# Optimization experiments

Hardware: AMD Instinct MI355X
Metric: run time of the kernel (lower is better)

Reference implementation:

```python
import jax, jax.numpy as jnp
import numpy as np

B, DIM, H, W = 8, 64, 128, 128
HEADS = 8
HID = DIM * 2          # ffn_expansion_factor = 2
DCONV = DIM // 4       # partial-conv channels
EPS_LN = 1e-5
EPS_NRM = 1e-12

def _conv(x, w, groups=1):
    # stride-1 conv, SAME padding (matches padding=1 for k=3, padding=0 for k=1)
    return jax.lax.conv_general_dilated(
        x, w, (1, 1), 'SAME',
        dimension_numbers=('NCHW', 'OIHW', 'NCHW'),
        feature_group_count=groups)

def _ln_channel(x, w, b):
    # WithBias LayerNorm over channel dim (to_3d puts c last, normalize last dim)
    mu = x.mean(axis=1, keepdims=True)
    var = ((x - mu) ** 2).mean(axis=1, keepdims=True)
    return (x - mu) / jnp.sqrt(var + EPS_LN) * w[None, :, None, None] + b[None, :, None, None]

def setup_inputs() -> dict:
    key = jax.random.key(0)
    ks = jax.random.split(key, 8)
    s = 0.02
    return {
        'x': jax.random.normal(ks[0], (B, DIM, H, W), jnp.float32),
        'ln1_w': jnp.ones((DIM,), jnp.float32),
        'ln1_b': jnp.zeros((DIM,), jnp.float32),
        'qkv_w': jax.random.normal(ks[1], (3 * DIM, DIM, 1, 1), jnp.float32) * s,
        'qkv_dw_w': jax.random.normal(ks[2], (3 * DIM, 1, 3, 3), jnp.float32) * s,
        'temperature': jnp.ones((HEADS, 1, 1), jnp.float32),
        'attn_mix': jnp.ones((2,), jnp.float32),
        'proj_w': jax.random.normal(ks[3], (DIM, DIM, 1, 1), jnp.float32) * s,
        'ln2_w': jnp.ones((DIM,), jnp.float32),
        'ln2_b': jnp.zeros((DIM,), jnp.float32),
        'pconv_w': jax.random.normal(ks[4], (DCONV, DCONV, 3, 3), jnp.float32) * s,
        'pin_w': jax.random.normal(ks[5], (2 * HID, DIM, 1, 1), jnp.float32) * s,
        'dw_w': jax.random.normal(ks[6], (HID, 1, 3, 3), jnp.float32) * s,
        'pout_w': jax.random.normal(ks[7], (DIM, HID, 1, 1), jnp.float32) * s,
    }

def reference(x, ln1_w, ln1_b, qkv_w, qkv_dw_w, temperature, attn_mix,
              proj_w, ln2_w, ln2_b, pconv_w, pin_w, dw_w, pout_w):
    b, c, h, w = x.shape
    ch = c // HEADS
    # ---- TwinPeakAttention on norm1(x) ----
    y = _ln_channel(x, ln1_w, ln1_b)
    qkv = _conv(_conv(y, qkv_w), qkv_dw_w, groups=3 * c)
    q, k, v = jnp.split(qkv, 3, axis=1)
    rs = lambda t: t.reshape(b, HEADS, ch, h * w)          # b head c (h w)
    q, k, v = rs(q), rs(k), rs(v)
    q = q / jnp.maximum(jnp.linalg.norm(q, axis=-1, keepdims=True), EPS_NRM)
    k = k / jnp.maximum(jnp.linalg.norm(k, axis=-1, keepdims=True), EPS_NRM)
    scores = jnp.einsum('bhcn,bhdn->bhcd', q, k)           # [b, head, ch, ch]
    attn_sm = jax.nn.softmax(scores * temperature[None], axis=-1)
    attn_relu = jnp.maximum(scores, 0.0) ** 2
    wmix = jax.nn.softmax(attn_mix)
    attn = wmix[0] * attn_sm + wmix[1] * attn_relu
    out = jnp.einsum('bhcd,bhdn->bhcn', attn, v).reshape(b, c, h, w)
    x = x + _conv(out, proj_w)
    # ---- FDFN on norm2(x) ----
    y = _ln_channel(x, ln2_w, ln2_b)
    y = jnp.concatenate([_conv(y[:, :DCONV], pconv_w), y[:, DCONV:]], axis=1)
    y = _conv(y, pin_w)                                    # [b, 2*HID, h, w]
    a, g = jnp.split(y, 2, axis=1)
    a = _conv(a, dw_w, groups=HID)
    y = _conv(jax.nn.gelu(a, approximate=False) * g, pout_w)
    return x + y
```

## Files before the change

kernel.cpp:

```cpp
#include <hip/hip_runtime.h>
#include <math.h>

#define NPIX 16384
#define B_ 8

typedef __attribute__((ext_vector_type(4))) float f32x4;
typedef __attribute__((ext_vector_type(8))) short bf16x8;
typedef __attribute__((ext_vector_type(4))) unsigned int u32x4;

__device__ inline unsigned short f2bf(float f) {
  unsigned int u = __builtin_bit_cast(unsigned int, f);
  return (unsigned short)((u + 0x7fffu + ((u >> 16) & 1u)) >> 16);
}
__device__ inline float bf2f(unsigned short h) {
  unsigned int u = ((unsigned int)h) << 16;
  return __builtin_bit_cast(float, u);
}
__device__ inline unsigned int pack2(unsigned short a, unsigned short b) {
  return (unsigned int)a | ((unsigned int)b << 16);
}
__device__ inline f32x4 mfma16(bf16x8 a, bf16x8 b, f32x4 c) {
  return __builtin_amdgcn_mfma_f32_16x16x32_bf16(a, b, c, 0, 0, 0);
}
__device__ inline void unpack8(u32x4 u, float* f) {
#pragma unroll
  for (int i = 0; i < 4; ++i) {
    unsigned int w = u[i];
    f[2 * i]     = __builtin_bit_cast(float, w << 16);
    f[2 * i + 1] = __builtin_bit_cast(float, w & 0xffff0000u);
  }
}


__global__ __launch_bounds__(256) void k0_prep(
    const float* __restrict__ wq, const float* __restrict__ lw,
    const float* __restrict__ lb, const float* __restrict__ pin,
    const float* __restrict__ pout, unsigned short* __restrict__ wq2,
    float* __restrict__ s1, float* __restrict__ s2,
    unsigned short* __restrict__ pinb, unsigned short* __restrict__ pob) {
  int bid = blockIdx.x, t = threadIdx.x;
  if (bid == 0) {
    if (t < 192) {
      int co = t;
      float a = 0.f, bsum = 0.f;
      for (int ci = 0; ci < 64; ++ci) {
        float w = wq[co * 64 + ci];
        unsigned short hb = f2bf(w * lw[ci]);
        wq2[co * 64 + ci] = hb;
        a += bf2f(hb);
        bsum = fmaf(w, lb[ci], bsum);
      }
      s1[co] = a;
      s2[co] = bsum;
    }
  } else if (bid <= 64) {
    int i = (bid - 1) * 256 + t;
    pinb[i] = f2bf(pin[i]);
  } else {
    int i = (bid - 65) * 256 + t;
    pob[i] = f2bf(pout[i]);
  }
}

__global__ __launch_bounds__(256) void k1_qkv(
    const float* __restrict__ x, const unsigned short* __restrict__ wq2,
    const float* __restrict__ s1, const float* __restrict__ s2,
    unsigned short* __restrict__ qkv) {
  __shared__ __align__(16) unsigned char lx[64 * 128];
  __shared__ float sumL[4][64], sqL[4][64], muL[64], rsL[64];
  __shared__ __align__(16) unsigned short epi[4][16][72];
  int t = threadIdx.x, blk = blockIdx.x;
  int b = blk >> 8, hw0 = (blk & 255) * 64;
  const float* xb = x + (size_t)b * 64 * NPIX + hw0;
  int p = t & 63, g8 = t >> 6;
  float psum = 0.f, psq = 0.f;
#pragma unroll
  for (int r = 0; r < 2; ++r) {
    int ci0 = g8 * 8 + r * 32;
    float v[8];
#pragma unroll
    for (int j = 0; j < 8; ++j) {
      v[j] = xb[(size_t)(ci0 + j) * NPIX + p];
      psum += v[j];
      psq = fmaf(v[j], v[j], psq);
    }
    u32x4 pk;
#pragma unroll
    for (int j = 0; j < 4; ++j) pk[j] = pack2(f2bf(v[2 * j]), f2bf(v[2 * j + 1]));
    unsigned int addr = ((unsigned)(p * 128 + ci0 * 2)) ^ ((p & 7) << 4);
    *(u32x4*)&lx[addr] = pk;
  }
  sumL[g8][p] = psum;
  sqL[g8][p] = psq;
  __syncthreads();
  if (t < 64) {
    float s = sumL[0][t] + sumL[1][t] + sumL[2][t] + sumL[3][t];
    float q = sqL[0][t] + sqL[1][t] + sqL[2][t] + sqL[3][t];
    float mu = s * (1.f / 64.f);
    float var = q * (1.f / 64.f) - mu * mu;
    muL[t] = mu;
    rsL[t] = rsqrtf(fmaxf(var, 0.f) + 1e-5f);
  }
  __syncthreads();
  int lane = t & 63, wv = t >> 6, l16 = lane & 15, g = lane >> 4;
  int co0 = wv * 48;
  bf16x8 A[3][2];
#pragma unroll
  for (int ct = 0; ct < 3; ++ct) {
    int co = co0 + ct * 16 + l16;
#pragma unroll
    for (int kh = 0; kh < 2; ++kh)
      A[ct][kh] = *(const bf16x8*)(wq2 + (size_t)co * 64 + kh * 32 + g * 8);
  }
  f32x4 acc[3][4];
#pragma unroll
  for (int ct = 0; ct < 3; ++ct)
#pragma unroll
    for (int nt = 0; nt < 4; ++nt) acc[ct][nt] = (f32x4)0.f;
#pragma unroll
  for (int nt = 0; nt < 4; ++nt) {
    int pp = nt * 16 + l16;
#pragma unroll
    for (int kh = 0; kh < 2; ++kh) {
      unsigned int addr = ((unsigned)(pp * 128 + (kh * 32 + g * 8) * 2)) ^ ((pp & 7) << 4);
      bf16x8 Bf = *(const bf16x8*)&lx[addr];
#pragma unroll
      for (int ct = 0; ct < 3; ++ct) acc[ct][nt] = mfma16(A[ct][kh], Bf, acc[ct][nt]);
    }
  }
  int row1 = hw0 >> 7, wb1 = hw0 & 127;
  unsigned short* ob = qkv + ((size_t)(b * 128 + row1) * 192) * 128 + wb1;
#pragma unroll
  for (int ct = 0; ct < 3; ++ct) {
#pragma unroll
    for (int r = 0; r < 4; ++r) {
      int co = co0 + ct * 16 + g * 4 + r;
      float s1v = s1[co], s2v = s2[co];
#pragma unroll
      for (int nt = 0; nt < 4; ++nt) {
        int pl = nt * 16 + l16;
        float val = (acc[ct][nt][r] - muL[pl] * s1v) * rsL[pl] + s2v;
        epi[wv][g * 4 + r][pl] = f2bf(val);
      }
    }
#pragma unroll
    for (int i = 0; i < 2; ++i) {
      int chunk = i * 64 + lane, co_l = chunk >> 3, oct = chunk & 7;
      u32x4 v = *(const u32x4*)&epi[wv][co_l][oct * 8];
      *(u32x4*)(ob + (size_t)(co0 + ct * 16 + co_l) * 128 + oct * 8) = v;
    }
  }
}

__global__ __launch_bounds__(256) void k2_dw3x3(
    const unsigned short* __restrict__ in, const float* __restrict__ w9,
    unsigned short* __restrict__ out) {
  int blk0 = blockIdx.x;
  int blk = (blk0 & 7) * 1536 + (blk0 >> 3);
  int id = blk * 256 + threadIdx.x;
  int oct = id & 15;
  int cr = id >> 4;
  int ch = cr % 192;
  int br = cr / 192;
  int row = br & 127;
  int w0 = oct * 8;
  const float* wp = w9 + ch * 9;
  float wgt[9];
#pragma unroll
  for (int j = 0; j < 9; ++j) wgt[j] = wp[j];
  float rowv[3][10];
#pragma unroll
  for (int dy = 0; dy < 3; ++dy) {
#pragma unroll
    for (int i = 0; i < 10; ++i) rowv[dy][i] = 0.f;
    int hh = row + dy - 1;
    if ((unsigned)hh < 128u) {
      const unsigned short* rp = in + ((size_t)(br + dy - 1) * 192 + ch) * 128 + w0;
      u32x4 m = *(const u32x4*)rp;
      unpack8(m, &rowv[dy][1]);
      if (w0 > 0) rowv[dy][0] = bf2f(rp[-1]);
      if (w0 < 120) rowv[dy][9] = bf2f(rp[8]);
    }
  }
  u32x4 res;
#pragma unroll
  for (int i = 0; i < 8; i += 2) {
    float a0 = 0.f, a1 = 0.f;
#pragma unroll
    for (int dy = 0; dy < 3; ++dy)
#pragma unroll
      for (int dx = 0; dx < 3; ++dx) {
        a0 = fmaf(wgt[dy * 3 + dx], rowv[dy][i + dx], a0);
        a1 = fmaf(wgt[dy * 3 + dx], rowv[dy][i + 1 + dx], a1);
      }
    res[i >> 1] = pack2(f2bf(a0), f2bf(a1));
  }
  *(u32x4*)(out + ((size_t)br * 192 + ch) * 128 + w0) = res;
}

__global__ __launch_bounds__(256) void k3a_mfma(
    const unsigned short* __restrict__ qkvd, float* __restrict__ parts) {
  __shared__ float red[4][640];
  int blk = blockIdx.x;
  int b = blk >> 6, chunk = blk & 63;
  int t = threadIdx.x;
  int lane = t & 63, wv = t >> 6, l16 = lane & 15, g = lane >> 4;
  const unsigned short* bb = qkvd + (size_t)(b * 128) * 192 * 128;
  int n0 = chunk * 256 + wv * 64;
  f32x4 S[4], QQ[4], KK[4];
#pragma unroll
  for (int i = 0; i < 4; ++i) { S[i] = (f32x4)0.f; QQ[i] = (f32x4)0.f; KK[i] = (f32x4)0.f; }
#pragma unroll
  for (int ks = 0; ks < 2; ++ks) {
    int k0 = n0 + ks * 32 + g * 8;
    int r = k0 >> 7, w = k0 & 127;
    const unsigned short* rowb = bb + ((size_t)r * 192) * 128 + w;
    bf16x8 Q[4], K[4];
#pragma unroll
    for (int t4 = 0; t4 < 4; ++t4) {
      Q[t4] = *(const bf16x8*)(rowb + (size_t)(t4 * 16 + l16) * 128);
      K[t4] = *(const bf16x8*)(rowb + (size_t)(64 + t4 * 16 + l16) * 128);
    }
#pragma unroll
    for (int t4 = 0; t4 < 4; ++t4) {
      S[t4]  = mfma16(Q[t4], K[t4], S[t4]);
      QQ[t4] = mfma16(Q[t4], Q[t4], QQ[t4]);
      KK[t4] = mfma16(K[t4], K[t4], KK[t4]);
    }
  }
  int hi = l16 >> 3;
#pragma unroll
  for (int t4 = 0; t4 < 4; ++t4) {
#pragma unroll
    for (int r = 0; r < 4; ++r) {
      int m = g * 4 + r;
      if ((m >> 3) == hi) {
        int head = 2 * t4 + hi;
        red[wv][head * 80 + 16 + (m & 7) * 8 + (l16 & 7)] = S[t4][r];
      }
      if (m == l16) {
        int c = t4 * 16 + l16;
        red[wv][(c >> 3) * 80 + (c & 7)] = QQ[t4][r];
        red[wv][(c >> 3) * 80 + 8 + (c & 7)] = KK[t4][r];
      }
    }
  }
  __syncthreads();
  float* pb = parts + (size_t)blk * 640;
  for (int i = t; i < 640; i += 256)
    pb[i] = red[0][i] + red[1][i] + red[2][i] + red[3][i];
}

__global__ __launch_bounds__(256) void k3bc(
    const float* __restrict__ parts, const float* __restrict__ temp,
    const float* __restrict__ mix, const float* __restrict__ pw,
    unsigned short* __restrict__ M) {
  int b = blockIdx.x, t = threadIdx.x;
  __shared__ float s[8][80];
  __shared__ float att[8][64];
  for (int i = t; i < 640; i += 256) {
    const float* pbase = parts + (size_t)b * 64 * 640 + i;
    float v = 0.f;
    for (int c = 0; c < 64; ++c) v += pbase[c * 640];
    s[i / 80][i % 80] = v;
  }
  __syncthreads();
  float m0 = fmaxf(mix[0], mix[1]);
  float e0 = expf(mix[0] - m0), e1 = expf(mix[1] - m0);
  float w0 = e0 / (e0 + e1), w1 = e1 / (e0 + e1);
  for (int i = t; i < 512; i += 256) {
    int head = i >> 6, e = i & 63, c = e >> 3, d = e & 7;
    float tt = temp[head];
    float rq = 1.f / fmaxf(sqrtf(s[head][c]), 1e-12f);
    float sc[8];
    float mx = -1e30f;
#pragma unroll
    for (int d2 = 0; d2 < 8; ++d2) {
      float rk = 1.f / fmaxf(sqrtf(s[head][8 + d2]), 1e-12f);
      sc[d2] = s[head][16 + c * 8 + d2] * rq * rk;
      mx = fmaxf(mx, sc[d2] * tt);
    }
    float sum = 0.f;
#pragma unroll
    for (int d2 = 0; d2 < 8; ++d2) sum += expf(sc[d2] * tt - mx);
    float sm = expf(sc[d] * tt - mx) / sum;
    float r = fmaxf(sc[d], 0.f);
    r = r * r;
    att[head][e] = w0 * sm + w1 * r;
  }
  __syncthreads();
  for (int i = t; i < 4096; i += 256) {
    int co = i >> 6, ci = i & 63, head = ci >> 3, d = ci & 7;
    float a = 0.f;
#pragma unroll
    for (int cc = 0; cc < 8; ++cc)
      a = fmaf(pw[co * 64 + head * 8 + cc], att[head][cc * 8 + d], a);
    M[(size_t)b * 4096 + i] = f2bf(a);
  }
}

__global__ __launch_bounds__(256) void k4_av(
    const unsigned short* __restrict__ qkvd, const unsigned short* __restrict__ Mb,
    const float* __restrict__ x, const float* __restrict__ lw,
    const float* __restrict__ lb, unsigned short* __restrict__ x1,
    unsigned short* __restrict__ y2) {
  __shared__ __align__(16) unsigned char lv[64 * 128];
  __shared__ float sumL[4][64], sqL[4][64], muL[64], rsL[64];
  int t = threadIdx.x, blk = blockIdx.x;
  int b = blk >> 8, hw0 = (blk & 255) * 64;
  int row4 = hw0 >> 7, wb4 = hw0 & 127;
  const unsigned short* vb = qkvd + ((size_t)(b * 128 + row4) * 192 + 128) * 128 + wb4;
  int p = t & 63, g8 = t >> 6;
#pragma unroll
  for (int r = 0; r < 2; ++r) {
    int ci0 = g8 * 8 + r * 32;
    unsigned short hh[8];
#pragma unroll
    for (int j = 0; j < 8; ++j) hh[j] = vb[(size_t)(ci0 + j) * 128 + p];
    u32x4 pk;
#pragma unroll
    for (int j = 0; j < 4; ++j) pk[j] = pack2(hh[2 * j], hh[2 * j + 1]);
    unsigned int addr = ((unsigned)(p * 128 + ci0 * 2)) ^ ((p & 7) << 4);
    *(u32x4*)&lv[addr] = pk;
  }
  __syncthreads();
  int lane = t & 63, wv = t >> 6, l16 = lane & 15, g = lane >> 4;
  bf16x8 A[2];
#pragma unroll
  for (int kh = 0; kh < 2; ++kh)
    A[kh] = *(const bf16x8*)(Mb + (size_t)b * 4096 + (size_t)(wv * 16 + l16) * 64 + kh * 32 + g * 8);
  f32x4 acc[4];
#pragma unroll
  for (int nt = 0; nt < 4; ++nt) acc[nt] = (f32x4)0.f;
#pragma unroll
  for (int nt = 0; nt < 4; ++nt) {
    int pp = nt * 16 + l16;
#pragma unroll
    for (int kh = 0; kh < 2; ++kh) {
      unsigned int addr = ((unsigned)(pp * 128 + (kh * 32 + g * 8) * 2)) ^ ((pp & 7) << 4);
      bf16x8 Bf = *(const bf16x8*)&lv[addr];
      acc[nt] = mfma16(A[kh], Bf, acc[nt]);
    }
  }
  const float* xb = x + (size_t)b * 64 * NPIX + hw0;
  unsigned short* x1b = x1 + (size_t)b * 64 * NPIX + hw0;
  float vals[4][4];
#pragma unroll
  for (int nt = 0; nt < 4; ++nt) {
    float ps = 0.f, pq = 0.f;
#pragma unroll
    for (int r = 0; r < 4; ++r) {
      int co = wv * 16 + g * 4 + r;
      size_t idx = (size_t)co * NPIX + nt * 16 + l16;
      float a = acc[nt][r] + xb[idx];
      vals[nt][r] = a;
      x1b[idx] = f2bf(a);
      ps += a;
      pq = fmaf(a, a, pq);
    }
    ps += __shfl_xor(ps, 16); ps += __shfl_xor(ps, 32);
    pq += __shfl_xor(pq, 16); pq += __shfl_xor(pq, 32);
    if (g == 0) { sumL[wv][nt * 16 + l16] = ps; sqL[wv][nt * 16 + l16] = pq; }
  }
  __syncthreads();
  if (t < 64) {
    float s = sumL[0][t] + sumL[1][t] + sumL[2][t] + sumL[3][t];
    float q = sqL[0][t] + sqL[1][t] + sqL[2][t] + sqL[3][t];
    float mu = s * (1.f / 64.f);
    float var = q * (1.f / 64.f) - mu * mu;
    muL[t] = mu;
    rsL[t] = rsqrtf(fmaxf(var, 0.f) + 1e-5f);
  }
  __syncthreads();
  unsigned short* y2b = y2 + (size_t)b * 64 * NPIX + hw0;
#pragma unroll
  for (int nt = 0; nt < 4; ++nt)
#pragma unroll
    for (int r = 0; r < 4; ++r) {
      int co = wv * 16 + g * 4 + r;
      int pl = nt * 16 + l16;
      float yv = (vals[nt][r] - muL[pl]) * rsL[pl] * lw[co] + lb[co];
      y2b[(size_t)co * NPIX + pl] = f2bf(yv);
    }
}

__global__ __launch_bounds__(256) void k5_pconv(
    const unsigned short* __restrict__ y2, const float* __restrict__ pcw,
    unsigned short* __restrict__ pc) {
  __shared__ unsigned short ly[16 * 120];
  int t = threadIdx.x, blk = blockIdx.x;
  int b = blk >> 8, tile = blk & 255;
  int ty = tile >> 4, tx = tile & 15;
  int h0 = ty * 8, w0 = tx * 8;
  const unsigned short* yb = y2 + (size_t)b * 64 * NPIX;
  for (int i = t; i < 1600; i += 256) {
    int ci = i / 100, r = i - ci * 100;
    int hy = r / 10, hx = r - hy * 10;
    int gh = h0 - 1 + hy, gw = w0 - 1 + hx;
    unsigned short v = 0;
    if ((unsigned)gh < 128u && (unsigned)gw < 128u) v = yb[(size_t)ci * NPIX + gh * 128 + gw];
    ly[ci * 120 + hy * 12 + hx] = v;
  }
  __syncthreads();
  int lp = t & 63;
  int py = lp >> 3, px = lp & 7;
  int cq = __builtin_amdgcn_readfirstlane(t >> 6);
  int co0 = cq * 4;
  float a0 = 0.f, a1 = 0.f, a2 = 0.f, a3 = 0.f;
  for (int ci = 0; ci < 16; ++ci) {
    float nb[9];
#pragma unroll
    for (int ky = 0; ky < 3; ++ky)
#pragma unroll
      for (int kx = 0; kx < 3; ++kx)
        nb[ky * 3 + kx] = bf2f(ly[ci * 120 + (py + ky) * 12 + px + kx]);
    const float* wp = pcw + (co0 * 16 + ci) * 9;
#pragma unroll
    for (int k = 0; k < 9; ++k) {
      a0 = fmaf(wp[k],       nb[k], a0);
      a1 = fmaf(wp[144 + k], nb[k], a1);
      a2 = fmaf(wp[288 + k], nb[k], a2);
      a3 = fmaf(wp[432 + k], nb[k], a3);
    }
  }
  size_t obase = (size_t)b * 16 * NPIX + (h0 + py) * 128 + w0 + px;
  pc[obase + (size_t)(co0 + 0) * NPIX] = f2bf(a0);
  pc[obase + (size_t)(co0 + 1) * NPIX] = f2bf(a1);
  pc[obase + (size_t)(co0 + 2) * NPIX] = f2bf(a2);
  pc[obase + (size_t)(co0 + 3) * NPIX] = f2bf(a3);
}

__global__ __launch_bounds__(256) void k6_pin(
    const unsigned short* __restrict__ pc, const unsigned short* __restrict__ y2,
    const unsigned short* __restrict__ pinb, unsigned short* __restrict__ ag) {
  __shared__ __align__(16) unsigned char bt[64 * 128];
  __shared__ __align__(16) unsigned short epi[4][16][72];
  int t = threadIdx.x, blk = blockIdx.x;
  int b = blk >> 8, hw0 = (blk & 255) * 64;
  int px = t & 63, cb = t >> 6;
  {
    const unsigned short* base = (cb == 0) ? (pc + (size_t)b * 16 * NPIX)
                                           : (y2 + (size_t)b * 64 * NPIX);
#pragma unroll
    for (int j = 0; j < 16; j += 2) {
      int ch = cb * 16 + j;
      unsigned short v0 = base[(size_t)ch * NPIX + hw0 + px];
      unsigned short v1 = base[(size_t)(ch + 1) * NPIX + hw0 + px];
      unsigned int addr = ((unsigned)(px * 128 + ch * 2)) ^ ((px & 7) << 4);
      *(unsigned int*)&bt[addr] = pack2(v0, v1);
    }
  }
  __syncthreads();
  int lane = t & 63, wv = t >> 6, l16 = lane & 15, g = lane >> 4;
  bf16x8 A[4][2];
#pragma unroll
  for (int ct = 0; ct < 4; ++ct) {
    int co = wv * 64 + ct * 16 + l16;
#pragma unroll
    for (int kh = 0; kh < 2; ++kh)
      A[ct][kh] = *(const bf16x8*)(pinb + (size_t)co * 64 + kh * 32 + g * 8);
  }
  f32x4 acc[4][4];
#pragma unroll
  for (int ct = 0; ct < 4; ++ct)
#pragma unroll
    for (int nt = 0; nt < 4; ++nt) acc[ct][nt] = (f32x4)0.f;
#pragma unroll
  for (int nt = 0; nt < 4; ++nt) {
    int pp = nt * 16 + l16;
#pragma unroll
    for (int kh = 0; kh < 2; ++kh) {
      unsigned int addr = ((unsigned)(pp * 128 + (kh * 32 + g * 8) * 2)) ^ ((pp & 7) << 4);
      bf16x8 Bf = *(const bf16x8*)&bt[addr];
#pragma unroll
      for (int ct = 0; ct < 4; ++ct) acc[ct][nt] = mfma16(A[ct][kh], Bf, acc[ct][nt]);
    }
  }
  int row6 = hw0 >> 7, wb6 = hw0 & 127;
  unsigned short* ab = ag + ((size_t)(b * 128 + row6) * 256) * 128 + wb6;
#pragma unroll
  for (int ct = 0; ct < 4; ++ct) {
#pragma unroll
    for (int nt = 0; nt < 4; ++nt)
#pragma unroll
      for (int r = 0; r < 4; ++r)
        epi[wv][g * 4 + r][nt * 16 + l16] = f2bf(acc[ct][nt][r]);
#pragma unroll
    for (int i = 0; i < 2; ++i) {
      int chunk = i * 64 + lane, co_l = chunk >> 3, oct = chunk & 7;
      u32x4 v = *(const u32x4*)&epi[wv][co_l][oct * 8];
      int co = wv * 64 + ct * 16 + co_l;
      *(u32x4*)(ab + (size_t)co * 128 + oct * 8) = v;
    }
  }
}

__global__ __launch_bounds__(256) void k7_fdfn(
    const unsigned short* __restrict__ ag, const float* __restrict__ dww,
    const unsigned short* __restrict__ pob, const unsigned short* __restrict__ x1,
    float* __restrict__ out) {
  __shared__ __align__(16) unsigned char bt[32 * 256];
  __shared__ float dwl[1152];
  int t = threadIdx.x;
  int blk0 = blockIdx.x;
  int blk = (blk0 & 7) * 512 + (blk0 >> 3);
  int b = blk >> 9, rr = blk & 511;
  int row = rr >> 2, w0t = (rr & 3) * 32;
  for (int i = t; i < 1152; i += 256) dwl[i] = dww[i];

  int chp = t >> 2, oct = t & 3;
  int ch0 = chp * 2;
  int w0 = w0t + oct * 8;
  bool hasL = (w0 > 0), hasR = (w0 < 120);
  u32x4 arow[2][3];
  u32x4 grow[2];
  unsigned short eL[2][3], eR[2][3];
#pragma unroll
  for (int cc = 0; cc < 2; ++cc) {
    int ch = ch0 + cc;
    grow[cc] = *(const u32x4*)(ag + ((size_t)(b * 128 + row) * 256 + 128 + ch) * 128 + w0);
#pragma unroll
    for (int dy = 0; dy < 3; ++dy) {
      int hh = row + dy - 1;
      bool v = (unsigned)hh < 128u;
      const unsigned short* rp = ag + ((size_t)(b * 128 + hh) * 256 + ch) * 128 + w0;
      arow[cc][dy] = v ? *(const u32x4*)rp : (u32x4)0u;
      eL[cc][dy] = (v && hasL) ? rp[-1] : (unsigned short)0;
      eR[cc][dy] = (v && hasR) ? rp[8] : (unsigned short)0;
    }
  }
  __syncthreads();

  {
    unsigned short hv[2][8];
#pragma unroll
    for (int cc = 0; cc < 2; ++cc) {
      float rowa[3][10], gt[8];
#pragma unroll
      for (int dy = 0; dy < 3; ++dy) {
        rowa[dy][0] = bf2f(eL[cc][dy]);
        unpack8(arow[cc][dy], &rowa[dy][1]);
        rowa[dy][9] = bf2f(eR[cc][dy]);
      }
      unpack8(grow[cc], gt);
      float wgt[9];
#pragma unroll
      for (int j = 0; j < 9; ++j) wgt[j] = dwl[(ch0 + cc) * 9 + j];
#pragma unroll
      for (int i2 = 0; i2 < 8; ++i2) {
        float a = 0.f;
#pragma unroll
        for (int dy = 0; dy < 3; ++dy)
#pragma unroll
          for (int dx = 0; dx < 3; ++dx)
            a = fmaf(wgt[dy * 3 + dx], rowa[dy][i2 + dx], a);
        float gl = 0.5f * a * (1.f + erff(a * 0.70710678118654752f)) * gt[i2];
        hv[cc][i2] = f2bf(gl);
      }
    }
#pragma unroll
    for (int i2 = 0; i2 < 8; ++i2) {
      int pxl = oct * 8 + i2;
      unsigned int f = (unsigned)(((pxl & 7) ^ (pxl >> 3)) << 4);
      unsigned int addr = (unsigned)(pxl * 256) + (((unsigned)(ch0 * 2)) ^ f);
      *(unsigned int*)&bt[addr] = pack2(hv[0][i2], hv[1][i2]);
    }
  }
  __syncthreads();
  int lane = t & 63, wv = t >> 6, l16 = lane & 15, g = lane >> 4;
  bf16x8 A[4];
#pragma unroll
  for (int kh = 0; kh < 4; ++kh)
    A[kh] = *(const bf16x8*)(pob + (size_t)(wv * 16 + l16) * 128 + kh * 32 + g * 8);
  f32x4 acc[2];
#pragma unroll
  for (int nt = 0; nt < 2; ++nt) acc[nt] = (f32x4)0.f;
#pragma unroll
  for (int nt = 0; nt < 2; ++nt) {
    int pp = nt * 16 + l16;
    unsigned int f = (unsigned)(((pp & 7) ^ (pp >> 3)) << 4);
#pragma unroll
    for (int kh = 0; kh < 4; ++kh) {
      unsigned int addr = (unsigned)(pp * 256) + (((unsigned)((kh * 32 + g * 8) * 2)) ^ f);
      bf16x8 Bf = *(const bf16x8*)&bt[addr];
      acc[nt] = mfma16(A[kh], Bf, acc[nt]);
    }
  }
  __syncthreads();
  float* ebuf = (float*)&bt[wv * 2048];
#pragma unroll
  for (int nt = 0; nt < 2; ++nt)
#pragma unroll
    for (int r = 0; r < 4; ++r)
      ebuf[(g * 4 + r) * 32 + nt * 16 + l16] = acc[nt][r];
  const unsigned short* x1b = x1 + (size_t)b * 64 * NPIX + row * 128 + w0t;
  float* ob = out + (size_t)b * 64 * NPIX + row * 128 + w0t;
#pragma unroll
  for (int i = 0; i < 2; ++i) {
    int chunk = i * 64 + lane;
    int co_l = chunk >> 3, q4 = (chunk & 7) * 4;
    f32x4 v = *(const f32x4*)&ebuf[co_l * 32 + q4];
    int co = wv * 16 + co_l;
    uint2 xv = *(const uint2*)(x1b + (size_t)co * NPIX + q4);
    f32x4 o;
    o[0] = v[0] + bf2f((unsigned short)(xv.x & 0xffffu));
    o[1] = v[1] + bf2f((unsigned short)(xv.x >> 16));
    o[2] = v[2] + bf2f((unsigned short)(xv.y & 0xffffu));
    o[3] = v[3] + bf2f((unsigned short)(xv.y >> 16));
    *(f32x4*)(ob + (size_t)co * NPIX + q4) = o;
  }
}

extern "C" void kernel_launch(void* const* d_in, const int* in_sizes, int n_in,
                              void* d_out, int out_size, void* d_ws, size_t ws_size,
                              hipStream_t stream) {
  const float* x       = (const float*)d_in[0];
  const float* ln1_w   = (const float*)d_in[1];
  const float* ln1_b   = (const float*)d_in[2];
  const float* qkv_w   = (const float*)d_in[3];
  const float* qkv_dww = (const float*)d_in[4];
  const float* temp    = (const float*)d_in[5];
  const float* mix     = (const float*)d_in[6];
  const float* proj_w  = (const float*)d_in[7];
  const float* ln2_w   = (const float*)d_in[8];
  const float* ln2_b   = (const float*)d_in[9];
  const float* pconv_w = (const float*)d_in[10];
  const float* pin_w   = (const float*)d_in[11];
  const float* dw_w    = (const float*)d_in[12];
  const float* pout_w  = (const float*)d_in[13];
  float* out = (float*)d_out;

  if (ws_size < (size_t)117515776) return;
  char* w8 = (char*)d_ws;
  unsigned short* qkv  = (unsigned short*)(w8 + 0);
  unsigned short* qkvd = (unsigned short*)(w8 + 50331648);
  unsigned short* x1   = (unsigned short*)(w8 + 100663296);
  unsigned short* wq2  = (unsigned short*)(w8 + 117440512);
  float*          s1   = (float*)(w8 + 117465088);
  float*          s2   = (float*)(w8 + 117465856);
  unsigned short* pinb = (unsigned short*)(w8 + 117466624);
  unsigned short* pob  = (unsigned short*)(w8 + 117499392);
  float*          parts= (float*)(w8 + 0);
  unsigned short* M    = (unsigned short*)(w8 + 2097152);
  unsigned short* y2   = (unsigned short*)(w8 + 4194304);
  unsigned short* pc   = (unsigned short*)(w8 + 20971520);
  unsigned short* ag   = (unsigned short*)(w8 + 33554432);

  k0_prep<<<97, 256, 0, stream>>>(qkv_w, ln1_w, ln1_b, pin_w, pout_w, wq2, s1, s2, pinb, pob);
  k1_qkv<<<2048, 256, 0, stream>>>(x, wq2, s1, s2, qkv);
  k2_dw3x3<<<12288, 256, 0, stream>>>(qkv, qkv_dww, qkvd);
  k3a_mfma<<<512, 256, 0, stream>>>(qkvd, parts);
  k3bc<<<8, 256, 0, stream>>>(parts, temp, mix, proj_w, M);
  k4_av<<<2048, 256, 0, stream>>>(qkvd, M, x, ln2_w, ln2_b, x1, y2);
  k5_pconv<<<2048, 256, 0, stream>>>(y2, pconv_w, pc);
  k6_pin<<<2048, 256, 0, stream>>>(pc, y2, pinb, ag);
  k7_fdfn<<<4096, 256, 0, stream>>>(ag, dw_w, pob, x1, out);
}
```

Before: 184.9 us.

## Stage k4 outputs through LDS for vector stores; widen k7 tiles to 64 pixels

In k4_av, the bf16 x1 and y2 outputs were written as scattered 2-byte stores. They are now staged in a padded LDS epilogue buffer and written back as 16-byte rows per channel. k7_fdfn moves to 512-thread blocks covering 64 pixels per row, with eight waves split across output-channel tiles and pixel halves. This halves the grid and amortizes the depthwise weight load. The cost is more LDS per block and possibly lower occupancy for k7.

```diff
diff --git a/kernel.cpp b/kernel.cpp
--- a/kernel.cpp
+++ b/kernel.cpp
@@ -306,6 +306,7 @@
     unsigned short* __restrict__ y2) {
   __shared__ __align__(16) unsigned char lv[64 * 128];
   __shared__ float sumL[4][64], sqL[4][64], muL[64], rsL[64];
+  __shared__ __align__(16) unsigned short epi[4][16][72];
   int t = threadIdx.x, blk = blockIdx.x;
   int b = blk >> 8, hw0 = (blk & 255) * 64;
   int row4 = hw0 >> 7, wb4 = hw0 & 127;
@@ -354,13 +355,19 @@
       size_t idx = (size_t)co * NPIX + nt * 16 + l16;
       float a = acc[nt][r] + xb[idx];
       vals[nt][r] = a;
-      x1b[idx] = f2bf(a);
+      epi[wv][g * 4 + r][nt * 16 + l16] = f2bf(a);
       ps += a;
       pq = fmaf(a, a, pq);
     }
     ps += __shfl_xor(ps, 16); ps += __shfl_xor(ps, 32);
     pq += __shfl_xor(pq, 16); pq += __shfl_xor(pq, 32);
     if (g == 0) { sumL[wv][nt * 16 + l16] = ps; sqL[wv][nt * 16 + l16] = pq; }
+  }
+#pragma unroll
+  for (int i = 0; i < 2; ++i) {
+    int chunk = i * 64 + lane, co_l = chunk >> 3, oct = chunk & 7;
+    u32x4 v = *(const u32x4*)&epi[wv][co_l][oct * 8];
+    *(u32x4*)(x1b + (size_t)(wv * 16 + co_l) * NPIX + oct * 8) = v;
   }
   __syncthreads();
   if (t < 64) {
@@ -380,8 +387,14 @@
       int co = wv * 16 + g * 4 + r;
       int pl = nt * 16 + l16;
       float yv = (vals[nt][r] - muL[pl]) * rsL[pl] * lw[co] + lb[co];
-      y2b[(size_t)co * NPIX + pl] = f2bf(yv);
-    }
+      epi[wv][g * 4 + r][pl] = f2bf(yv);
+    }
+#pragma unroll
+  for (int i = 0; i < 2; ++i) {
+    int chunk = i * 64 + lane, co_l = chunk >> 3, oct = chunk & 7;
+    u32x4 v = *(const u32x4*)&epi[wv][co_l][oct * 8];
+    *(u32x4*)(y2b + (size_t)(wv * 16 + co_l) * NPIX + oct * 8) = v;
+  }
 }
 
 __global__ __launch_bounds__(256) void k5_pconv(
@@ -495,20 +508,20 @@
   }
 }
 
-__global__ __launch_bounds__(256) void k7_fdfn(
+__global__ __launch_bounds__(512) void k7_fdfn(
     const unsigned short* __restrict__ ag, const float* __restrict__ dww,
     const unsigned short* __restrict__ pob, const unsigned short* __restrict__ x1,
     float* __restrict__ out) {
-  __shared__ __align__(16) unsigned char bt[32 * 256];
+  __shared__ __align__(16) unsigned char bt[64 * 256];
   __shared__ float dwl[1152];
   int t = threadIdx.x;
   int blk0 = blockIdx.x;
-  int blk = (blk0 & 7) * 512 + (blk0 >> 3);
-  int b = blk >> 9, rr = blk & 511;
-  int row = rr >> 2, w0t = (rr & 3) * 32;
-  for (int i = t; i < 1152; i += 256) dwl[i] = dww[i];
-
-  int chp = t >> 2, oct = t & 3;
+  int blk = (blk0 & 7) * 256 + (blk0 >> 3);
+  int b = blk >> 8, rr = blk & 255;
+  int row = rr >> 1, w0t = (rr & 1) * 64;
+  for (int i = t; i < 1152; i += 512) dwl[i] = dww[i];
+
+  int chp = t >> 3, oct = t & 7;
   int ch0 = chp * 2;
   int w0 = w0t + oct * 8;
   bool hasL = (w0 > 0), hasR = (w0 < 120);
@@ -554,8 +567,8 @@
 #pragma unroll
           for (int dx = 0; dx < 3; ++dx)
             a = fmaf(wgt[dy * 3 + dx], rowa[dy][i2 + dx], a);
-        float gl = 0.5f * a * (1.f + erff(a * 0.70710678118654752f)) * gt[i2];
-        hv[cc][i2] = f2bf(gl);
+        float gl = 0.5f * a * (1.f + erff(a * 0.70710678118654752f));
+        hv[cc][i2] = f2bf(gl * gt[i2]);
       }
     }
 #pragma unroll
@@ -568,39 +581,42 @@
   }
   __syncthreads();
   int lane = t & 63, wv = t >> 6, l16 = lane & 15, g = lane >> 4;
+  int cot = wv >> 1;
+  int pxh = (wv & 1) * 2;
   bf16x8 A[4];
 #pragma unroll
   for (int kh = 0; kh < 4; ++kh)
-    A[kh] = *(const bf16x8*)(pob + (size_t)(wv * 16 + l16) * 128 + kh * 32 + g * 8);
+    A[kh] = *(const bf16x8*)(pob + (size_t)(cot * 16 + l16) * 128 + kh * 32 + g * 8);
   f32x4 acc[2];
 #pragma unroll
-  for (int nt = 0; nt < 2; ++nt) acc[nt] = (f32x4)0.f;
-#pragma unroll
-  for (int nt = 0; nt < 2; ++nt) {
-    int pp = nt * 16 + l16;
+  for (int j = 0; j < 2; ++j) acc[j] = (f32x4)0.f;
+#pragma unroll
+  for (int j = 0; j < 2; ++j) {
+    int pp = (pxh + j) * 16 + l16;
     unsigned int f = (unsigned)(((pp & 7) ^ (pp >> 3)) << 4);
 #pragma unroll
     for (int kh = 0; kh < 4; ++kh) {
       unsigned int addr = (unsigned)(pp * 256) + (((unsigned)((kh * 32 + g * 8) * 2)) ^ f);
       bf16x8 Bf = *(const bf16x8*)&bt[addr];
-      acc[nt] = mfma16(A[kh], Bf, acc[nt]);
+      acc[j] = mfma16(A[kh], Bf, acc[j]);
     }
   }
   __syncthreads();
   float* ebuf = (float*)&bt[wv * 2048];
 #pragma unroll
-  for (int nt = 0; nt < 2; ++nt)
+  for (int j = 0; j < 2; ++j)
 #pragma unroll
     for (int r = 0; r < 4; ++r)
-      ebuf[(g * 4 + r) * 32 + nt * 16 + l16] = acc[nt][r];
-  const unsigned short* x1b = x1 + (size_t)b * 64 * NPIX + row * 128 + w0t;
-  float* ob = out + (size_t)b * 64 * NPIX + row * 128 + w0t;
+      ebuf[(g * 4 + r) * 32 + j * 16 + l16] = acc[j][r];
+  int pxb = (wv & 1) * 32;
+  const unsigned short* x1b = x1 + (size_t)b * 64 * NPIX + row * 128 + w0t + pxb;
+  float* ob = out + (size_t)b * 64 * NPIX + row * 128 + w0t + pxb;
 #pragma unroll
   for (int i = 0; i < 2; ++i) {
     int chunk = i * 64 + lane;
     int co_l = chunk >> 3, q4 = (chunk & 7) * 4;
     f32x4 v = *(const f32x4*)&ebuf[co_l * 32 + q4];
-    int co = wv * 16 + co_l;
+    int co = cot * 16 + co_l;
     uint2 xv = *(const uint2*)(x1b + (size_t)co * NPIX + q4);
     f32x4 o;
     o[0] = v[0] + bf2f((unsigned short)(xv.x & 0xffffu));
@@ -654,5 +670,5 @@
   k4_av<<<2048, 256, 0, stream>>>(qkvd, M, x, ln2_w, ln2_b, x1, y2);
   k5_pconv<<<2048, 256, 0, stream>>>(y2, pconv_w, pc);
   k6_pin<<<2048, 256, 0, stream>>>(pc, y2, pinb, ag);
-  k7_fdfn<<<4096, 256, 0, stream>>>(ag, dw_w, pob, x1, out);
-}
+  k7_fdfn<<<2048, 512, 0, stream>>>(ag, dw_w, pob, x1, out);
+}
```

Measured after the change: 175.5 us. 5.1% less time.
